# Performance work log

Measured on AMD Instinct MI355X. Metric: run time of the kernel, lower is better.

## Reference

```python
import jax, jax.numpy as jnp
import numpy as np

SCALE = 1
L = 16          # level_num
THETA = 0.5
EPS = 1e-6
BN_EPS = 1e-5
C_IN = 16       # out_chan(144) - 128


def setup_inputs() -> dict:
    key = jax.random.key(0)
    ks = jax.random.split(key, 8)
    init = lambda k, shape, fan_in: jax.random.normal(k, shape, jnp.float32) * (1.0 / np.sqrt(fan_in))
    d = {}
    d["x"] = jax.random.normal(ks[0], (4, C_IN, 256, 256), jnp.float32)
    # 1x1 convs stored as (out_ch, in_ch) matrices
    d["f1_w"] = init(ks[1], (64, 3), 3);        d["f1_b"] = jnp.zeros((64,), jnp.float32)
    d["f2_w"] = init(ks[2], (128, 64), 64);     d["f2_b"] = jnp.zeros((128,), jnp.float32)
    d["o1_w"] = init(ks[3], (128, 144), 144);   d["o1_b"] = jnp.zeros((128,), jnp.float32)
    d["bn1_g"] = jnp.ones((128,), jnp.float32); d["bn1_b"] = jnp.zeros((128,), jnp.float32)
    d["o2_w"] = init(ks[4], (128, 128), 128);   d["o2_b"] = jnp.zeros((128,), jnp.float32)
    d["bn2_g"] = jnp.ones((128,), jnp.float32); d["bn2_b"] = jnp.zeros((128,), jnp.float32)
    return d


def _bn_train(x, g, b):
    # torch BatchNorm2d in training mode: biased batch stats over (N, spatial)
    m = x.mean(axis=(0, 2), keepdims=True)
    v = ((x - m) ** 2).mean(axis=(0, 2), keepdims=True)
    return g[None, :, None] * (x - m) / jnp.sqrt(v + BN_EPS) + b[None, :, None]


def _conv1x1(w, b, x):  # x: (N, Cin, P) -> (N, Cout, P)
    return jnp.einsum('oc,ncp->nop', w, x) + b[None, :, None]


def reference(x, f1_w, f1_b, f2_w, f2_b, o1_w, o1_b, bn1_g, bn1_b, o2_w, o2_b, bn2_g, bn2_b):
    N, C, H, W = x.shape
    # global average feature (adaptive_avg_pool2d to (1,1), upsampled back = broadcast)
    mu = x.mean(axis=(2, 3), keepdims=True)                       # (N,C,1,1)
    xn = x / jnp.maximum(jnp.linalg.norm(x, axis=1, keepdims=True), 1e-12)
    mn = mu / jnp.maximum(jnp.linalg.norm(mu, axis=1, keepdims=True), 1e-12)
    cos = (xn * mn).sum(1)                                        # (N,H,W)
    cosf = cos.reshape(N, H * W)
    cmin = cosf.min(axis=1, keepdims=True)                        # (N,1)
    cmax = cosf.max(axis=1, keepdims=True)
    q = (2.0 * jnp.arange(L, dtype=x.dtype) + 1.0) / (2.0 * L) * (cmax - cmin) + cmin  # (N,L)
    sigma = 2.0 / L
    # soft gaussian binning: (N,H,W,L)
    quant = jnp.exp(-(cos[..., None] - q[:, None, None, :]) ** 2 / (2.0 * sigma ** 2))
    qp = jnp.transpose(quant, (0, 3, 1, 2))                       # (N,L,H,W)
    qp = jnp.pad(qp, ((0, 0), (0, 0), (0, 1), (0, 1)))            # pad right/bottom with 0
    left = qp[:, :, :H, :W]                                       # (N,L,H,W)
    right = qp[:, :, 1:, 1:]                                      # (N,L,H,W) diagonal neighbor
    co = left[:, :, None, :, :] * right[:, None, :, :, :]         # (N,L,L,H,W) co-occurrence
    co = (co - co.min()) / (co.max() - co.min() + EPS)            # global min-max normalize
    sta = co.sum(axis=(-1, -2))                                   # (N,L,L)
    # features: [q broadcast along rows, q broadcast along cols, sta]
    q_h = jnp.broadcast_to(q[:, None, :], (N, L, L))
    q_w = jnp.broadcast_to(q[:, :, None], (N, L, L))
    feat = jnp.stack([q_h, q_w, sta], axis=1).reshape(N, 3, L * L)
    h = jax.nn.leaky_relu(_conv1x1(f1_w, f1_b, feat), 0.01)       # f1
    h = jax.nn.relu(_conv1x1(f2_w, f2_b, h))                      # f2
    xav = jnp.broadcast_to(mu.reshape(N, C, 1), (N, C, L * L))
    h = jnp.concatenate([xav, h], axis=1)                         # (N,144,L^2)
    h = jax.nn.relu(_bn_train(_conv1x1(o1_w, o1_b, h), bn1_g, bn1_b))
    h = _bn_train(_conv1x1(o2_w, o2_b, h), bn2_g, bn2_b)
    s = h.mean(-1).reshape(N, 128, SCALE, SCALE)
    # denoise: redistribute energy above theta*max
    mx = s.max()
    extra = jnp.sum(jnp.maximum(s - THETA * mx, 0.0))
    r = extra / L
    de = jnp.where(s > THETA * mx, THETA * mx + r, s + r)
    de = (de - de.min()) / (de.max() - de.min() + EPS)
    return de
```

## Files before the change

### kernel.cpp

```cpp
#include <hip/hip_runtime.h>
#include <math.h>

#define W_MUP2  0
#define W_LOP   1024
#define W_HIP   2048
#define W_CMXP  3072
#define W_BN1F  3584
#define W_O1T   3840
#define W_O2T   22272
#define W_COS   38912
#define W_GP    (W_COS + 262144)
#define W_RAW   (W_GP + 131072)
#define W_BN1P  (W_RAW + 131072)
#define W_BN2P  (W_BN1P + 65536)

__device__ __forceinline__ float wrSum(float v){
#pragma unroll
  for(int o = 32; o > 0; o >>= 1) v += __shfl_down(v, o, 64);
  return v;
}
__device__ __forceinline__ float wrSumX(float v){
#pragma unroll
  for(int o = 32; o > 0; o >>= 1) v += __shfl_xor(v, o, 64);
  return v;
}
__device__ __forceinline__ float wrMax(float v){
#pragma unroll
  for(int o = 32; o > 0; o >>= 1) v = fmaxf(v, __shfl_down(v, o, 64));
  return v;
}
__device__ __forceinline__ float wrMin(float v){
#pragma unroll
  for(int o = 32; o > 0; o >>= 1) v = fminf(v, __shfl_down(v, o, 64));
  return v;
}

__global__ __launch_bounds__(256)
void k_mu(const float* __restrict__ x, const float* __restrict__ o1w,
          const float* __restrict__ o2w, float* __restrict__ ws){
  const int t = threadIdx.x, b = blockIdx.x;
  if(b < 1024){
    __shared__ float red[4];
    const float4* xb = (const float4*)(x + b*4096);
    float4 v0 = xb[t], v1 = xb[t+256], v2 = xb[t+512], v3 = xb[t+768];
    float s = ((v0.x+v0.y)+(v0.z+v0.w)) + ((v1.x+v1.y)+(v1.z+v1.w))
            + ((v2.x+v2.y)+(v2.z+v2.w)) + ((v3.x+v3.y)+(v3.z+v3.w));
    s = wrSum(s);
    if((t & 63) == 0) red[t>>6] = s;
    __syncthreads();
    if(t == 0) ws[W_MUP2 + b] = (red[0]+red[1])+(red[2]+red[3]);
  } else if(b < 1042){
    const int c0 = (b - 1024)*8;
#pragma unroll
    for(int j = 0; j < 4; ++j){
      int idx = t + j*256;
      int ch = idx & 127, c = c0 + (idx >> 7);
      if(c < 144) ws[W_O1T + c*128 + ch] = o1w[ch*144 + c];
    }
  } else {
    const int c0 = (b - 1042)*8;
#pragma unroll
    for(int j = 0; j < 4; ++j){
      int idx = t + j*256;
      int ch = idx & 127, c = c0 + (idx >> 7);
      ws[W_O2T + c*128 + ch] = o2w[ch*128 + c];
    }
  }
}

__global__ __launch_bounds__(256)
void k_cos(const float* __restrict__ x, float* __restrict__ ws){
  __shared__ float sp[256];
  __shared__ float mu[16];
  __shared__ float red[8];
  const int t = threadIdx.x, b = blockIdx.x;
  const int n = b >> 8, p = (b & 255)*256 + t;
  sp[t] = ws[W_MUP2 + n*256 + t];
  __syncthreads();
  if(t < 16){
    float m = 0.0f;
#pragma unroll
    for(int q = 0; q < 16; ++q) m += sp[t*16 + q];
    mu[t] = m * (1.0f/65536.0f);
  }
  __syncthreads();
  float nn = 0.0f;
#pragma unroll
  for(int c = 0; c < 16; ++c) nn += mu[c]*mu[c];
  const float inv = 1.0f / fmaxf(sqrtf(nn), 1e-12f);
  const float* xp = x + n*1048576 + p;
  float dot = 0.0f, xx = 0.0f;
#pragma unroll
  for(int c = 0; c < 16; ++c){ float v = xp[c*65536]; dot += v*mu[c]; xx += v*v; }
  const float cv = dot * inv / fmaxf(sqrtf(xx), 1e-12f);
  ws[W_COS + n*65536 + p] = cv;
  float lo = wrMin(cv), hi = wrMax(cv);
  if((t & 63) == 0){ red[t>>6] = lo; red[4 + (t>>6)] = hi; }
  __syncthreads();
  if(t == 0){
    ws[W_LOP + b] = fminf(fminf(red[0],red[1]),fminf(red[2],red[3]));
    ws[W_HIP + b] = fmaxf(fmaxf(red[4],red[5]),fmaxf(red[6],red[7]));
  }
}

__global__ __launch_bounds__(256) void k_gram(float* __restrict__ ws){
  __shared__ __align__(16) float smem[10256];
  float* Lsh = smem;
  float* Rsh = smem + 5120;
  const int t = threadIdx.x, b = blockIdx.x;
  const int n = b >> 7, h0 = (b & 127) << 1;
  {
    float lo = ws[W_LOP + n*256 + t];
    float hi = ws[W_HIP + n*256 + t];
    lo = wrMin(lo); hi = wrMax(hi);
    if((t & 63) == 0){ smem[10240 + (t>>6)] = lo; smem[10244 + (t>>6)] = hi; }
  }
  __syncthreads();
  const float cmin = fminf(fminf(smem[10240],smem[10241]),fminf(smem[10242],smem[10243]));
  const float cmax = fmaxf(fmaxf(smem[10244],smem[10245]),fmaxf(smem[10246],smem[10247]));
  const float dqv  = cmax - cmin;
  float q[16];
#pragma unroll
  for(int l = 0; l < 16; ++l) q[l] = (float)(2*l+1) * (1.0f/32.0f) * dqv + cmin;

  const int m  = t & 15;
  const int g  = t >> 4;
  const int i0 = (m >> 2) << 2;
  const int j0 = (m & 3) << 2;
  float acc[4][4] = {{0.0f}};
  float mp = 0.0f;
  const float* cosp = ws + W_COS + n*65536;

  __syncthreads();
#pragma unroll
  for(int ch = 0; ch < 2; ++ch){
    const int h = h0 + ch;
    const float cl = cosp[h*256 + t];
    const bool valid = (h < 255) && (t < 255);
    const float cr = valid ? cosp[h*256 + t + 257] : 0.0f;
    float lv[16], rv[16];
    float mL = 0.0f, mR = 0.0f;
#pragma unroll
    for(int l = 0; l < 16; ++l){
      float dl = cl - q[l];
      float Lv = __expf(-32.0f * dl * dl);
      float dr = cr - q[l];
      float Rv = valid ? __expf(-32.0f * dr * dr) : 0.0f;
      lv[l] = Lv; rv[l] = Rv;
      mL = fmaxf(mL, Lv); mR = fmaxf(mR, Rv);
    }
    mp = fmaxf(mp, mL * mR);
    float4* Lp = (float4*)&Lsh[t * 20];
    float4* Rp = (float4*)&Rsh[t * 20];
#pragma unroll
    for(int k = 0; k < 4; ++k){
      Lp[k] = make_float4(lv[4*k], lv[4*k+1], lv[4*k+2], lv[4*k+3]);
      Rp[k] = make_float4(rv[4*k], rv[4*k+1], rv[4*k+2], rv[4*k+3]);
    }
    __syncthreads();
#pragma unroll 4
    for(int it = 0; it < 16; ++it){
      const int p = it * 16 + g;
      const float4 Lx = *(const float4*)&Lsh[p*20 + i0];
      const float4 Rx = *(const float4*)&Rsh[p*20 + j0];
      const float lf[4] = {Lx.x, Lx.y, Lx.z, Lx.w};
      const float rf[4] = {Rx.x, Rx.y, Rx.z, Rx.w};
#pragma unroll
      for(int a = 0; a < 4; ++a)
#pragma unroll
        for(int bb = 0; bb < 4; ++bb) acc[a][bb] += lf[a] * rf[bb];
    }
    __syncthreads();
  }
#pragma unroll
  for(int a = 0; a < 4; ++a)
#pragma unroll
    for(int bb = 0; bb < 4; ++bb)
      Lsh[t*16 + a*4 + bb] = acc[a][bb];
  __syncthreads();
  const int i = t >> 4, j = t & 15;
  const int mm = ((i >> 2) << 2) + (j >> 2);
  const int idx = mm*16 + (i & 3)*4 + (j & 3);
  float v = 0.0f;
#pragma unroll
  for(int gg = 0; gg < 16; ++gg) v += Lsh[gg*256 + idx];
  ws[W_GP + b*256 + t] = v;

  mp = wrMax(mp);
  if((t & 63) == 0) smem[10240 + (t >> 6)] = mp;
  __syncthreads();
  if(t == 0)
    ws[W_CMXP + b] = fmaxf(fmaxf(smem[10240],smem[10241]),fmaxf(smem[10242],smem[10243]));
}

__global__ __launch_bounds__(256)
void k_mlp1(const float* __restrict__ f1w, const float* __restrict__ f1b,
            const float* __restrict__ f2w, const float* __restrict__ f2b,
            const float* __restrict__ o1b,
            float* __restrict__ ws)
{
  __shared__ __align__(16) float smem[10496];
  const int t = threadIdx.x, b = blockIdx.x;
  const int n = b >> 6, pos0 = (b & 63) << 2;

#pragma unroll
  for(int k = 0; k < 8; ++k){
    float4 v = ((const float4*)f2w)[k*256 + t];
    int e = (k*256 + t)*4;
    int ch = e >> 6, c = e & 63;
    smem[(c+0)*129 + ch] = v.x;
    smem[(c+1)*129 + ch] = v.y;
    smem[(c+2)*129 + ch] = v.z;
    smem[(c+3)*129 + ch] = v.w;
  }
  if(t < 192) smem[8256 + t] = f1w[t];
  if(t < 64)  smem[8448 + t] = f1b[t];
  {
    float m2 = fmaxf(ws[W_CMXP + t], ws[W_CMXP + 256 + t]);
    m2 = wrMax(m2);
    if((t & 63) == 0) smem[9536 + (t >> 6)] = m2;
  }
  {
    float lo = ws[W_LOP + n*256 + t];
    float hi = ws[W_HIP + n*256 + t];
    lo = wrMin(lo); hi = wrMax(hi);
    if((t & 63) == 0){ smem[9540 + (t>>6)] = lo; smem[9544 + (t>>6)] = hi; }
  }
  smem[10112 + t] = ws[W_MUP2 + n*256 + t];
  __syncthreads();
  if(t < 16){
    float m = 0.0f;
#pragma unroll
    for(int q = 0; q < 16; ++q) m += smem[10112 + t*16 + q];
    smem[9552 + t] = m * (1.0f/65536.0f);
  }
  const float comax = fmaxf(fmaxf(smem[9536],smem[9537]),fmaxf(smem[9538],smem[9539]));
  const float cmin  = fminf(fminf(smem[9540],smem[9541]),fminf(smem[9542],smem[9543]));
  const float cmax  = fmaxf(fmaxf(smem[9544],smem[9545]),fmaxf(smem[9546],smem[9547]));
  const float dqv   = cmax - cmin;
  const int w = t >> 6, j = t & 63;
  const int pos = pos0 + w;
  float gv = ws[W_GP + (n*128 + j)*256 + pos]
           + ws[W_GP + (n*128 + 64 + j)*256 + pos];
  gv = wrSumX(gv);
  const float sta = gv / (comax + 1e-6f);
  const int l1 = pos >> 4, l2 = pos & 15;
  const float ft0 = (float)(2*l2+1)*(1.0f/32.0f)*dqv + cmin;
  const float ft1 = (float)(2*l1+1)*(1.0f/32.0f)*dqv + cmin;
  float a = smem[8256+3*j]*ft0 + smem[8256+3*j+1]*ft1 + smem[8256+3*j+2]*sta + smem[8448+j];
  smem[8512 + w*64 + j] = (a > 0.0f) ? a : 0.01f*a;
  __syncthreads();
  {
    float acc0 = f2b[j], acc1 = f2b[j+64];
    const float* h1p = &smem[8512 + w*64];
#pragma unroll
    for(int c = 0; c < 64; ++c){
      float hv = h1p[c];
      acc0 += smem[c*129 + j]      * hv;
      acc1 += smem[c*129 + j + 64] * hv;
    }
    acc0 = fmaxf(acc0, 0.0f); acc1 = fmaxf(acc1, 0.0f);
    smem[8768 + j*6 + w]      = acc0;
    smem[8768 + (j+64)*6 + w] = acc1;
  }
  __syncthreads();
  {
    const int ch = t & 127, w2 = t >> 7;
    float base = o1b[ch];
#pragma unroll
    for(int c = 0; c < 16; ++c) base += ws[W_O1T + c*128 + ch] * smem[9552 + c];
#pragma unroll
    for(int k = 0; k < 2; ++k){
      const int ww = w2*2 + k;
      float v = base;
#pragma unroll 8
      for(int c = 0; c < 128; ++c) v += ws[W_O1T + (16 + c)*128 + ch] * smem[8768 + c*6 + ww];
      smem[9600 + ch*4 + ww] = v;
    }
  }
  __syncthreads();
  if(t < 128){
    float v0 = smem[9600 + t*4], v1 = smem[9600 + t*4 + 1];
    float v2 = smem[9600 + t*4 + 2], v3 = smem[9600 + t*4 + 3];
    *(float4*)(ws + W_RAW + n*32768 + t*256 + pos0) = make_float4(v0,v1,v2,v3);
    ws[W_BN1P + b*256 + t]       = (v0+v1)+(v2+v3);
    ws[W_BN1P + b*256 + 128 + t] = (v0*v0+v1*v1)+(v2*v2+v3*v3);
  }
}

__global__ __launch_bounds__(256)
void k_bn1(const float* __restrict__ g1, const float* __restrict__ b1,
           float* __restrict__ ws)
{
  __shared__ float col[256];
  const int t = threadIdx.x;
  float a0 = 0.0f, a1 = 0.0f, a2 = 0.0f, a3 = 0.0f;
  for(int k = 0; k < 256; k += 4){
    a0 += ws[W_BN1P + (k+0)*256 + t];
    a1 += ws[W_BN1P + (k+1)*256 + t];
    a2 += ws[W_BN1P + (k+2)*256 + t];
    a3 += ws[W_BN1P + (k+3)*256 + t];
  }
  col[t] = (a0+a1)+(a2+a3);
  __syncthreads();
  if(t < 128){
    float S = col[t], S2 = col[128 + t];
    float mean = S * (1.0f/1024.0f);
    float var  = S2 * (1.0f/1024.0f) - mean*mean;
    float sc = g1[t] * rsqrtf(var + 1e-5f);
    ws[W_BN1F + t]       = sc;
    ws[W_BN1F + 128 + t] = b1[t] - mean*sc;
  }
}

__global__ __launch_bounds__(256)
void k_mlp2(const float* __restrict__ o2b, float* __restrict__ ws)
{
  __shared__ __align__(16) float scsh[256];
  __shared__ __align__(16) float h3s[512];
  __shared__ __align__(16) float o2s[512];
  const int t = threadIdx.x, b = blockIdx.x;
  const int n = b >> 6, pos0 = (b & 63) << 2;

  scsh[t] = ws[W_BN1F + t];
  __syncthreads();
  if(t < 128){
    float4 rv = *(const float4*)(ws + W_RAW + n*32768 + t*256 + pos0);
    float sc = scsh[t], sh = scsh[128 + t];
    h3s[t*4+0] = fmaxf(rv.x*sc + sh, 0.0f);
    h3s[t*4+1] = fmaxf(rv.y*sc + sh, 0.0f);
    h3s[t*4+2] = fmaxf(rv.z*sc + sh, 0.0f);
    h3s[t*4+3] = fmaxf(rv.w*sc + sh, 0.0f);
  }
  __syncthreads();
  {
    const int ch = t & 127, w2 = t >> 7;
#pragma unroll
    for(int k = 0; k < 2; ++k){
      const int ww = w2*2 + k;
      float v = o2b[ch];
#pragma unroll 8
      for(int c = 0; c < 128; ++c) v += ws[W_O2T + c*128 + ch] * h3s[c*4 + ww];
      o2s[ch*4 + ww] = v;
    }
  }
  __syncthreads();
  if(t < 128){
    float a0 = o2s[t*4], a1 = o2s[t*4+1], a2 = o2s[t*4+2], a3 = o2s[t*4+3];
    ws[W_BN2P + b*256 + t]       = (a0+a1)+(a2+a3);
    ws[W_BN2P + b*256 + 128 + t] = (a0*a0+a1*a1)+(a2*a2+a3*a3);
  }
}

__global__ __launch_bounds__(256)
void k_fin(const float* __restrict__ g2, const float* __restrict__ b2,
           float* __restrict__ ws, float* __restrict__ out)
{
  __shared__ __align__(16) float sS[512];
  __shared__ float s2S[128];
  __shared__ float red[16];
  const int t = threadIdx.x;

  if(t < 128){
#pragma unroll
    for(int nn = 0; nn < 4; ++nn){
      float a = 0.0f;
      for(int k = 0; k < 64; ++k) a += ws[W_BN2P + (nn*64 + k)*256 + t];
      sS[nn*128 + t] = a;
    }
  }else{
    const int ch = t - 128;
    float a = 0.0f;
    for(int k = 0; k < 256; ++k) a += ws[W_BN2P + k*256 + 128 + ch];
    s2S[ch] = a;
  }
  __syncthreads();
  if(t < 128){
    float S = ((sS[t] + sS[128+t]) + (sS[256+t] + sS[384+t]));
    float S2 = s2S[t];
    float mean = S * (1.0f/1024.0f);
    float var  = S2 * (1.0f/1024.0f) - mean*mean;
    float sc = g2[t] * rsqrtf(var + 1e-5f);
    float sh = b2[t] - mean*sc;
#pragma unroll
    for(int nn = 0; nn < 4; ++nn)
      sS[nn*128 + t] = sS[nn*128 + t]*(1.0f/256.0f)*sc + sh;
  }
  __syncthreads();
  float v0 = sS[t], v1 = sS[256 + t];
  float m = fmaxf(v0, v1);
  m = wrMax(m);
  if((t & 63) == 0) red[t>>6] = m;
  __syncthreads();
  const float mx = fmaxf(fmaxf(red[0],red[1]),fmaxf(red[2],red[3]));
  const float thr = 0.5f * mx;
  float e = fmaxf(v0 - thr, 0.0f) + fmaxf(v1 - thr, 0.0f);
  e = wrSum(e);
  if((t & 63) == 0) red[4 + (t>>6)] = e;
  __syncthreads();
  const float r = (red[4]+red[5]+red[6]+red[7]) * (1.0f/16.0f);
  const float d0 = (v0 > thr) ? (thr + r) : (v0 + r);
  const float d1 = (v1 > thr) ? (thr + r) : (v1 + r);
  float dn = fminf(d0, d1), dx = fmaxf(d0, d1);
  dn = wrMin(dn); dx = wrMax(dx);
  if((t & 63) == 0){ red[8 + (t>>6)] = dn; red[12 + (t>>6)] = dx; }
  __syncthreads();
  const float DN = fminf(fminf(red[8],red[9]),fminf(red[10],red[11]));
  const float DX = fmaxf(fmaxf(red[12],red[13]),fmaxf(red[14],red[15]));
  const float inv = 1.0f / (DX - DN + 1e-6f);
  out[t]       = (d0 - DN) * inv;
  out[256 + t] = (d1 - DN) * inv;
}

extern "C" void kernel_launch(void* const* d_in, const int* in_sizes, int n_in,
                              void* d_out, int out_size, void* d_ws, size_t ws_size,
                              hipStream_t stream){
  (void)in_sizes; (void)n_in; (void)out_size; (void)ws_size;
  const float* x   = (const float*)d_in[0];
  const float* f1w = (const float*)d_in[1];
  const float* f1b = (const float*)d_in[2];
  const float* f2w = (const float*)d_in[3];
  const float* f2b = (const float*)d_in[4];
  const float* o1w = (const float*)d_in[5];
  const float* o1b = (const float*)d_in[6];
  const float* g1  = (const float*)d_in[7];
  const float* b1  = (const float*)d_in[8];
  const float* o2w = (const float*)d_in[9];
  const float* o2b = (const float*)d_in[10];
  const float* g2  = (const float*)d_in[11];
  const float* b2  = (const float*)d_in[12];
  float* ws  = (float*)d_ws;
  float* out = (float*)d_out;

  k_mu  <<<1058, 256, 0, stream>>>(x, o1w, o2w, ws);
  k_cos <<<1024, 256, 0, stream>>>(x, ws);
  k_gram<<<512,  256, 0, stream>>>(ws);
  k_mlp1<<<256,  256, 0, stream>>>(f1w, f1b, f2w, f2b, o1b, ws);
  k_bn1 <<<1,    256, 0, stream>>>(g1, b1, ws);
  k_mlp2<<<256,  256, 0, stream>>>(o2b, ws);
  k_fin <<<1,    256, 0, stream>>>(g2, b2, ws, out);
}
```

Measured before the change: 63.94 us.

## Fuse BN1 stats into mlp2, vectorize cos kernel, coalesce gram/raw accesses

Removes the single-block k_bn1 launch. Each k_mlp2 block now redundantly reduces the BN1 partial sums itself before normalizing. k_cos now handles two pixels per thread with float2 loads and half as many blocks, with the per-block min/max partials adjusted to match. k_mlp1 stages its gram partials through shared memory with float4 loads, and the RAW intermediate changes to a position-major layout so the stores and loads are coalesced. The trade is that every mlp2 block repeats the 256x256 partial reduction, in exchange for one fewer launch and its serialization point.

New measurement: 62.64 us, median of 2. -2.0%, faster.

```diff
diff --git a/kernel.cpp b/kernel.cpp
--- a/kernel.cpp
+++ b/kernel.cpp
@@ -5,7 +5,6 @@
 #define W_LOP   1024
 #define W_HIP   2048
 #define W_CMXP  3072
-#define W_BN1F  3584
 #define W_O1T   3840
 #define W_O2T   22272
 #define W_COS   38912
@@ -74,7 +73,7 @@
   __shared__ float mu[16];
   __shared__ float red[8];
   const int t = threadIdx.x, b = blockIdx.x;
-  const int n = b >> 8, p = (b & 255)*256 + t;
+  const int n = b >> 7, bb = b & 127;
   sp[t] = ws[W_MUP2 + n*256 + t];
   __syncthreads();
   if(t < 16){
@@ -88,18 +87,23 @@
 #pragma unroll
   for(int c = 0; c < 16; ++c) nn += mu[c]*mu[c];
   const float inv = 1.0f / fmaxf(sqrtf(nn), 1e-12f);
-  const float* xp = x + n*1048576 + p;
-  float dot = 0.0f, xx = 0.0f;
-#pragma unroll
-  for(int c = 0; c < 16; ++c){ float v = xp[c*65536]; dot += v*mu[c]; xx += v*v; }
-  const float cv = dot * inv / fmaxf(sqrtf(xx), 1e-12f);
-  ws[W_COS + n*65536 + p] = cv;
-  float lo = wrMin(cv), hi = wrMax(cv);
+  const float2* xp = (const float2*)(x + n*1048576 + bb*512) + t;
+  float dot0 = 0.0f, xx0 = 0.0f, dot1 = 0.0f, xx1 = 0.0f;
+#pragma unroll
+  for(int c = 0; c < 16; ++c){
+    float2 v = xp[c*32768];
+    dot0 += v.x*mu[c]; xx0 += v.x*v.x;
+    dot1 += v.y*mu[c]; xx1 += v.y*v.y;
+  }
+  const float cv0 = dot0 * inv / fmaxf(sqrtf(xx0), 1e-12f);
+  const float cv1 = dot1 * inv / fmaxf(sqrtf(xx1), 1e-12f);
+  *(float2*)(ws + W_COS + n*65536 + bb*512 + 2*t) = make_float2(cv0, cv1);
+  float lo = wrMin(fminf(cv0, cv1)), hi = wrMax(fmaxf(cv0, cv1));
   if((t & 63) == 0){ red[t>>6] = lo; red[4 + (t>>6)] = hi; }
   __syncthreads();
   if(t == 0){
-    ws[W_LOP + b] = fminf(fminf(red[0],red[1]),fminf(red[2],red[3]));
-    ws[W_HIP + b] = fmaxf(fmaxf(red[4],red[5]),fmaxf(red[6],red[7]));
+    ws[W_LOP + n*128 + bb] = fminf(fminf(red[0],red[1]),fminf(red[2],red[3]));
+    ws[W_HIP + n*128 + bb] = fmaxf(fmaxf(red[4],red[5]),fmaxf(red[6],red[7]));
   }
 }
 
@@ -110,8 +114,8 @@
   const int t = threadIdx.x, b = blockIdx.x;
   const int n = b >> 7, h0 = (b & 127) << 1;
   {
-    float lo = ws[W_LOP + n*256 + t];
-    float hi = ws[W_HIP + n*256 + t];
+    float lo = (t < 128) ? ws[W_LOP + n*128 + t] : 1e30f;
+    float hi = (t < 128) ? ws[W_HIP + n*128 + t] : -1e30f;
     lo = wrMin(lo); hi = wrMax(hi);
     if((t & 63) == 0){ smem[10240 + (t>>6)] = lo; smem[10244 + (t>>6)] = hi; }
   }
@@ -221,12 +225,19 @@
     if((t & 63) == 0) smem[9536 + (t >> 6)] = m2;
   }
   {
-    float lo = ws[W_LOP + n*256 + t];
-    float hi = ws[W_HIP + n*256 + t];
+    float lo = (t < 128) ? ws[W_LOP + n*128 + t] : 1e30f;
+    float hi = (t < 128) ? ws[W_HIP + n*128 + t] : -1e30f;
     lo = wrMin(lo); hi = wrMax(hi);
     if((t & 63) == 0){ smem[9540 + (t>>6)] = lo; smem[9544 + (t>>6)] = hi; }
   }
   smem[10112 + t] = ws[W_MUP2 + n*256 + t];
+  if(t < 128){
+    float4 gp = *(const float4*)(ws + W_GP + (n*128 + t)*256 + pos0);
+    smem[9600 + t]        = gp.x;
+    smem[9600 + 128 + t]  = gp.y;
+    smem[9600 + 256 + t]  = gp.z;
+    smem[9600 + 384 + t]  = gp.w;
+  }
   __syncthreads();
   if(t < 16){
     float m = 0.0f;
@@ -240,8 +251,7 @@
   const float dqv   = cmax - cmin;
   const int w = t >> 6, j = t & 63;
   const int pos = pos0 + w;
-  float gv = ws[W_GP + (n*128 + j)*256 + pos]
-           + ws[W_GP + (n*128 + 64 + j)*256 + pos];
+  float gv = smem[9600 + w*128 + j] + smem[9600 + w*128 + 64 + j];
   gv = wrSumX(gv);
   const float sta = gv / (comax + 1e-6f);
   const int l1 = pos >> 4, l2 = pos & 15;
@@ -279,58 +289,58 @@
     }
   }
   __syncthreads();
+  {
+    const int ch = t & 127, k = t >> 7;
+    ws[W_RAW + n*32768 + (pos0+k)*128 + ch]   = smem[9600 + ch*4 + k];
+    ws[W_RAW + n*32768 + (pos0+k+2)*128 + ch] = smem[9600 + ch*4 + k+2];
+  }
   if(t < 128){
     float v0 = smem[9600 + t*4], v1 = smem[9600 + t*4 + 1];
     float v2 = smem[9600 + t*4 + 2], v3 = smem[9600 + t*4 + 3];
-    *(float4*)(ws + W_RAW + n*32768 + t*256 + pos0) = make_float4(v0,v1,v2,v3);
     ws[W_BN1P + b*256 + t]       = (v0+v1)+(v2+v3);
     ws[W_BN1P + b*256 + 128 + t] = (v0*v0+v1*v1)+(v2*v2+v3*v3);
   }
 }
 
 __global__ __launch_bounds__(256)
-void k_bn1(const float* __restrict__ g1, const float* __restrict__ b1,
-           float* __restrict__ ws)
+void k_mlp2(const float* __restrict__ o2b,
+            const float* __restrict__ g1, const float* __restrict__ b1,
+            float* __restrict__ ws)
 {
   __shared__ float col[256];
-  const int t = threadIdx.x;
-  float a0 = 0.0f, a1 = 0.0f, a2 = 0.0f, a3 = 0.0f;
-  for(int k = 0; k < 256; k += 4){
-    a0 += ws[W_BN1P + (k+0)*256 + t];
-    a1 += ws[W_BN1P + (k+1)*256 + t];
-    a2 += ws[W_BN1P + (k+2)*256 + t];
-    a3 += ws[W_BN1P + (k+3)*256 + t];
-  }
-  col[t] = (a0+a1)+(a2+a3);
-  __syncthreads();
-  if(t < 128){
-    float S = col[t], S2 = col[128 + t];
-    float mean = S * (1.0f/1024.0f);
-    float var  = S2 * (1.0f/1024.0f) - mean*mean;
-    float sc = g1[t] * rsqrtf(var + 1e-5f);
-    ws[W_BN1F + t]       = sc;
-    ws[W_BN1F + 128 + t] = b1[t] - mean*sc;
-  }
-}
-
-__global__ __launch_bounds__(256)
-void k_mlp2(const float* __restrict__ o2b, float* __restrict__ ws)
-{
   __shared__ __align__(16) float scsh[256];
   __shared__ __align__(16) float h3s[512];
   __shared__ __align__(16) float o2s[512];
   const int t = threadIdx.x, b = blockIdx.x;
   const int n = b >> 6, pos0 = (b & 63) << 2;
 
-  scsh[t] = ws[W_BN1F + t];
-  __syncthreads();
-  if(t < 128){
-    float4 rv = *(const float4*)(ws + W_RAW + n*32768 + t*256 + pos0);
-    float sc = scsh[t], sh = scsh[128 + t];
-    h3s[t*4+0] = fmaxf(rv.x*sc + sh, 0.0f);
-    h3s[t*4+1] = fmaxf(rv.y*sc + sh, 0.0f);
-    h3s[t*4+2] = fmaxf(rv.z*sc + sh, 0.0f);
-    h3s[t*4+3] = fmaxf(rv.w*sc + sh, 0.0f);
+  {
+    float a0 = 0.0f, a1 = 0.0f, a2 = 0.0f, a3 = 0.0f;
+    for(int k = 0; k < 256; k += 4){
+      a0 += ws[W_BN1P + (k+0)*256 + t];
+      a1 += ws[W_BN1P + (k+1)*256 + t];
+      a2 += ws[W_BN1P + (k+2)*256 + t];
+      a3 += ws[W_BN1P + (k+3)*256 + t];
+    }
+    col[t] = (a0+a1)+(a2+a3);
+  }
+  __syncthreads();
+  if(t < 128){
+    float S = col[t], S2 = col[128 + t];
+    float mean = S * (1.0f/1024.0f);
+    float var  = S2 * (1.0f/1024.0f) - mean*mean;
+    float sc = g1[t] * rsqrtf(var + 1e-5f);
+    scsh[t]       = sc;
+    scsh[128 + t] = b1[t] - mean*sc;
+  }
+  __syncthreads();
+  {
+    const int ch = t & 127, k = t >> 7;
+    float sc = scsh[ch], sh = scsh[128 + ch];
+    float r0 = ws[W_RAW + n*32768 + (pos0+k)*128 + ch];
+    float r1 = ws[W_RAW + n*32768 + (pos0+k+2)*128 + ch];
+    h3s[ch*4 + k]   = fmaxf(r0*sc + sh, 0.0f);
+    h3s[ch*4 + k+2] = fmaxf(r1*sc + sh, 0.0f);
   }
   __syncthreads();
   {
@@ -433,10 +443,9 @@
   float* out = (float*)d_out;
 
   k_mu  <<<1058, 256, 0, stream>>>(x, o1w, o2w, ws);
-  k_cos <<<1024, 256, 0, stream>>>(x, ws);
+  k_cos <<<512,  256, 0, stream>>>(x, ws);
   k_gram<<<512,  256, 0, stream>>>(ws);
   k_mlp1<<<256,  256, 0, stream>>>(f1w, f1b, f2w, f2b, o1b, ws);
-  k_bn1 <<<1,    256, 0, stream>>>(g1, b1, ws);
-  k_mlp2<<<256,  256, 0, stream>>>(o2b, ws);
+  k_mlp2<<<256,  256, 0, stream>>>(o2b, g1, b1, ws);
   k_fin <<<1,    256, 0, stream>>>(g2, b2, ws, out);
 }
```
